# Kernel tuning notes

Measured on AMD Instinct MI355X. Metric: run time of the kernel, lower is better.

## Reference

```python
import jax, jax.numpy as jnp
import numpy as np

K = 20          # knn neighbors (args.k)
BN_EPS = 1e-5   # torch BatchNorm default
LN_EPS = 1e-6


def _bn(x, g, b, axes):
    # training-mode batchnorm over `axes`, channel dim = 1
    m = x.mean(axes, keepdims=True)
    v = x.var(axes, keepdims=True)
    shp = [1] * x.ndim
    shp[1] = x.shape[1]
    return g.reshape(shp) * (x - m) * jax.lax.rsqrt(v + BN_EPS) + b.reshape(shp)


def _lrelu(x):
    return jnp.where(x >= 0, x, 0.2 * x)


def _graph_feature(x, k):
    # x: [B,C,N] -> [B,2C,N,k]  (knn gather + (neighbor-center, center) concat)
    B, C, N = x.shape
    inner = -2.0 * jnp.einsum('bcn,bcm->bnm', x, x)
    xx = jnp.sum(x * x, axis=1)                       # [B,N]
    pd = -xx[:, :, None] - inner - xx[:, None, :]     # negative sq. distance
    idx = jax.lax.top_k(pd, k)[1]                     # [B,N,k]
    xt = jnp.transpose(x, (0, 2, 1))                  # [B,N,C]
    feat = xt[jnp.arange(B)[:, None, None], idx]      # [B,N,k,C] gather
    ctr = xt[:, :, None, :]
    out = jnp.concatenate([feat - ctr, jnp.broadcast_to(ctr, feat.shape)], axis=-1)
    return jnp.transpose(out, (0, 3, 1, 2))


def _conv2d_block(x, w, g, b):
    # 1x1 conv2d (no bias) + BN2d + LeakyReLU(0.2)
    y = jnp.einsum('bcnk,oc->bonk', x, w)
    return _lrelu(_bn(y, g, b, (0, 2, 3)))


def _conv1d_block(x, w, g, b):
    y = jnp.einsum('bcl,oc->bol', x, w)
    return _lrelu(_bn(y, g, b, (0, 2)))


def _squash(t):
    sn = jnp.sum(t * t, axis=-1, keepdims=True)
    return sn * t / ((1.0 + sn) * jnp.sqrt(sn))


def _forward(data, l, dw1, dg1, db1, dw2, dg2, db2, dw3, dg3, db3,
             lin_w, ln_w, ln_b, caps_W,
             cw1, cg1, cb1, cw2, cg2, cb2, cw3, cw4, cg4, cb4, cw5, cg5, cb5):
    B, _, N = data.shape
    # ---- DGCNN encoder ----
    x = _conv2d_block(_graph_feature(data, K), dw1, dg1, db1)
    x1 = x.max(axis=-1)                               # [B,64,N]
    x = _conv2d_block(_graph_feature(x1, K), dw2, dg2, db2)
    x2 = x.max(axis=-1)                               # [B,64,N]
    x = _conv2d_block(_graph_feature(x2, K), dw3, dg3, db3)
    x3 = x.max(axis=-1)                               # [B,128,N]
    feat = jnp.transpose(jnp.concatenate([x1, x2, x3], axis=1), (0, 2, 1))  # [B,N,256]
    h = jnp.einsum('bnc,oc->bno', feat, lin_w)        # [B,N,40]
    mu = h.mean(axis=(1, 2), keepdims=True)
    var = h.var(axis=(1, 2), keepdims=True)
    encoder = jax.nn.relu(ln_w * (h - mu) * jax.lax.rsqrt(var + LN_EPS) + ln_b)  # [B,1024,40]
    # ---- Latent capsule layer (3-iter dynamic routing) ----
    u_hat = jnp.einsum('lpvd,bpd->blpv', caps_W, encoder)  # [B,40,1024,64]
    u_det = jax.lax.stop_gradient(u_hat)
    b_ij = jnp.zeros((B, caps_W.shape[0], caps_W.shape[1]), encoder.dtype)
    v = None
    for it in range(3):
        c = jax.nn.softmax(b_ij, axis=1)
        if it == 2:
            v = _squash(jnp.einsum('blp,blpv->blv', c, u_hat))
        else:
            v = _squash(jnp.einsum('blp,blpv->blv', c, u_det))
            b_ij = b_ij + jnp.einsum('blv,blpv->blp', v, u_det)
    latent = v                                        # [B,40,64]
    # ---- segmentation head ----
    emb = jnp.einsum('bpd,bdv->bpv', encoder, latent) # [B,1024,64]
    emb = emb.max(axis=-1, keepdims=True)             # [B,1024,1]
    lab = _conv1d_block(l.reshape(B, -1, 1), cw1, cg1, cb1)  # [B,64,1]
    emb = jnp.concatenate([emb, lab], axis=1)         # [B,1088,1]
    emb = jnp.tile(emb, (1, 1, N))                    # [B,1088,N]
    emb = jnp.concatenate([emb, jnp.transpose(encoder, (0, 2, 1))], axis=1)  # [B,1128,N]
    r = _conv1d_block(emb, cw2, cg2, cb2)
    r = _conv1d_block(r, cw3, cg2, cb2)               # conv3 shares bn2 params
    r = _conv1d_block(r, cw4, cg4, cb4)
    r = _conv1d_block(r, cw5, cg5, cb5)
    return r                                          # [B,50,N]


def setup_inputs() -> dict:
    key = jax.random.key(0)
    ks = jax.random.split(key, 16)
    B, N = 32, 1024
    f = jnp.float32
    rn = lambda k, s: 0.05 * jax.random.normal(k, s, dtype=f)
    return dict(
        data=jax.random.normal(ks[0], (B, 3, N), dtype=f),
        l=jax.random.uniform(ks[1], (B, 16), dtype=f),
        dw1=rn(ks[2], (64, 6)), dg1=jnp.ones(64, f), db1=jnp.zeros(64, f),
        dw2=rn(ks[3], (64, 128)), dg2=jnp.ones(64, f), db2=jnp.zeros(64, f),
        dw3=rn(ks[4], (128, 128)), dg3=jnp.ones(128, f), db3=jnp.zeros(128, f),
        lin_w=rn(ks[5], (40, 256)),
        ln_w=jnp.ones((N, 40), f), ln_b=jnp.zeros((N, 40), f),
        caps_W=0.01 * jax.random.normal(ks[6], (40, 1024, 64, 40), dtype=f),
        cw1=rn(ks[7], (64, 16)), cg1=jnp.ones(64, f), cb1=jnp.zeros(64, f),
        cw2=rn(ks[8], (256, 1128)), cg2=jnp.ones(256, f), cb2=jnp.zeros(256, f),
        cw3=rn(ks[9], (256, 256)),
        cw4=rn(ks[10], (128, 256)), cg4=jnp.ones(128, f), cb4=jnp.zeros(128, f),
        cw5=rn(ks[11], (50, 128)), cg5=jnp.ones(50, f), cb5=jnp.zeros(50, f),
    )


def reference(data, l, dw1, dg1, db1, dw2, dg2, db2, dw3, dg3, db3,
              lin_w, ln_w, ln_b, caps_W,
              cw1, cg1, cb1, cw2, cg2, cb2, cw3, cw4, cg4, cb4, cw5, cg5, cb5):
    return _forward(data, l, dw1, dg1, db1, dw2, dg2, db2, dw3, dg3, db3,
                    lin_w, ln_w, ln_b, caps_W,
                    cw1, cg1, cb1, cw2, cg2, cb2, cw3, cw4, cg4, cb4, cw5, cg5, cb5)
```

## Files before the change

### kernel.cpp

```cpp
#include <hip/hip_runtime.h>
#include <math.h>

constexpr int NB = 32, NN = 1024, KNN = 20;
constexpr int RTOT = NB * NN;

constexpr size_t SZ_BIG = (size_t)NB * NN * 40 * 64;
constexpr size_t O_BIG  = 0;
constexpr size_t O_XT0  = O_BIG + SZ_BIG;
constexpr size_t O_XT1  = O_XT0 + (size_t)RTOT * 4;
constexpr size_t O_XT2  = O_XT1 + (size_t)RTOT * 64;
constexpr size_t O_XT3  = O_XT2 + (size_t)RTOT * 64;
constexpr size_t O_XX   = O_XT3 + (size_t)RTOT * 128;
constexpr size_t O_IDX  = O_XX + RTOT;
constexpr size_t O_WC1  = O_IDX + (size_t)RTOT * KNN;
constexpr size_t O_WC2  = O_WC1 + 512;
constexpr size_t O_WC3  = O_WC2 + 8192;
constexpr size_t O_LWT  = O_WC3 + 16384;
constexpr size_t O_C2T  = O_LWT + 16384;
constexpr size_t O_C3T  = O_C2T + 10240;
constexpr size_t O_C4T  = O_C3T + 65536;
constexpr size_t O_C5T  = O_C4T + 32768;
constexpr size_t O_H    = O_C5T + 8192;
constexpr size_t O_LNST = O_H + (size_t)RTOT * 64;
constexpr size_t O_BSUM = O_LNST + 64;
constexpr size_t O_BSQ  = O_BSUM + 256;
constexpr size_t O_SCL  = O_BSQ + 256;
constexpr size_t O_SHF  = O_SCL + 256;
constexpr size_t O_SACC = O_SHF + 256;
constexpr size_t O_VB   = O_SACC + 81920;
constexpr size_t O_BIJ  = O_VB + 81920;
constexpr size_t O_EMB  = O_BIJ + (size_t)NB * 40 * NN;
constexpr size_t O_LAB  = O_EMB + RTOT;
constexpr size_t O_BASE = O_LAB + 2048;
constexpr size_t O_PS   = O_BIJ;
constexpr size_t O_PQ   = O_BIJ + 262144;
constexpr size_t O_PB   = O_XT1;
constexpr size_t O_PBU  = O_XT1;

__device__ __forceinline__ float lrelu(float z) { return fmaxf(z, 0.2f * z); }

__device__ __forceinline__ float key2f(unsigned u)
{
    unsigned b = (u & 0x80000000u) ? (u ^ 0x80000000u) : ~u;
    return __uint_as_float(b);
}

__device__ __forceinline__ unsigned bfpack(float a, float b)
{
    unsigned ua = __float_as_uint(a); unsigned ub = __float_as_uint(b);
    ua += 0x7FFFu + ((ua >> 16) & 1u);
    ub += 0x7FFFu + ((ub >> 16) & 1u);
    return (ua >> 16) | (ub & 0xFFFF0000u);
}
__device__ __forceinline__ float bflo(unsigned u) { return __uint_as_float(u << 16); }
__device__ __forceinline__ float bfhi(unsigned u) { return __uint_as_float(u & 0xFFFF0000u); }

__device__ __forceinline__ void wt_do(const float* __restrict__ src, float* __restrict__ dst,
                                      int i, int K, int On, int SS, int coff, int DS, int ooff, int Oreal)
{
    if (i >= K * On) return;
    int c = i / On, o = i - c * On;
    dst[(size_t)c * DS + ooff + o] = (o < Oreal) ? src[(size_t)o * SS + coff + c] : 0.f;
}

__global__ __launch_bounds__(256) void k_wtall(
    const float* __restrict__ dw1, const float* __restrict__ dw2, const float* __restrict__ dw3,
    const float* __restrict__ lw,  const float* __restrict__ cw2, const float* __restrict__ cw3,
    const float* __restrict__ cw4, const float* __restrict__ cw5,
    float* __restrict__ wc1, float* __restrict__ wc2, float* __restrict__ wc3,
    float* __restrict__ lwt, float* __restrict__ c2t, float* __restrict__ c3t,
    float* __restrict__ c4t, float* __restrict__ c5t)
{
    int bid = blockIdx.x, t = threadIdx.x;
    if      (bid < 1)   wt_do(dw1, wc1, (bid - 0) * 256 + t,   3, 64, 6, 0, 128, 0, 64);
    else if (bid < 2)   wt_do(dw1, wc1, (bid - 1) * 256 + t,   3, 64, 6, 3, 128, 64, 64);
    else if (bid < 18)  wt_do(dw2, wc2, (bid - 2) * 256 + t,   64, 64, 128, 0, 128, 0, 64);
    else if (bid < 34)  wt_do(dw2, wc2, (bid - 18) * 256 + t,  64, 64, 128, 64, 128, 64, 64);
    else if (bid < 66)  wt_do(dw3, wc3, (bid - 34) * 256 + t,  64, 128, 128, 0, 256, 0, 128);
    else if (bid < 98)  wt_do(dw3, wc3, (bid - 66) * 256 + t,  64, 128, 128, 64, 256, 128, 128);
    else if (bid < 162) wt_do(lw,  lwt, (bid - 98) * 256 + t,  256, 64, 256, 0, 64, 0, 40);
    else if (bid < 202) wt_do(cw2, c2t, (bid - 162) * 256 + t, 40, 256, 1128, 1088, 256, 0, 256);
    else if (bid < 458) wt_do(cw3, c3t, (bid - 202) * 256 + t, 256, 256, 256, 0, 256, 0, 256);
    else if (bid < 586) wt_do(cw4, c4t, (bid - 458) * 256 + t, 256, 128, 256, 0, 128, 0, 128);
    else                wt_do(cw5, c5t, (bid - 586) * 256 + t, 128, 64, 128, 0, 64, 0, 50);
}

__global__ void k_data_t(const float* __restrict__ d, float* __restrict__ xt,
                         float* __restrict__ xx)
{
    int i = blockIdx.x * 256 + threadIdx.x;
    if (i >= RTOT) return;
    int b = i >> 10, n = i & 1023;
    float s = 0.f;
#pragma unroll
    for (int c = 0; c < 3; ++c) {
        float v = d[((size_t)b * 3 + c) * NN + n];
        xt[(size_t)i * 4 + c] = v;
        s = fmaf(v, v, s);
    }
    xt[(size_t)i * 4 + 3] = 0.f;
    xx[i] = s;
}

template<int CS>
__global__ __launch_bounds__(256) void k_dist(const float* __restrict__ X,
    const float* __restrict__ xx, float* __restrict__ D)
{
    __shared__ float As[16][68];
    __shared__ float Bs[16][68];
    int b = blockIdx.z;
    int r0 = blockIdx.x * 64, m0 = blockIdx.y * 64;
    const float* Xb = X + (size_t)b * NN * CS;
    int t = threadIdx.x;
    int tx = t & 15, ty = t >> 4;
    float acc[4][4] = {};
    for (int k0 = 0; k0 < CS; k0 += 16) {
        __syncthreads();
        {
            int row = t >> 2, kb = (t & 3) * 4;
            float4 a4 = make_float4(0.f, 0.f, 0.f, 0.f);
            float4 b4 = make_float4(0.f, 0.f, 0.f, 0.f);
            if (k0 + kb < CS) {
                a4 = *(const float4*)&Xb[(size_t)(r0 + row) * CS + k0 + kb];
                b4 = *(const float4*)&Xb[(size_t)(m0 + row) * CS + k0 + kb];
            }
            As[kb + 0][row] = a4.x; As[kb + 1][row] = a4.y;
            As[kb + 2][row] = a4.z; As[kb + 3][row] = a4.w;
            Bs[kb + 0][row] = b4.x; Bs[kb + 1][row] = b4.y;
            Bs[kb + 2][row] = b4.z; Bs[kb + 3][row] = b4.w;
        }
        __syncthreads();
#pragma unroll
        for (int k = 0; k < 16; ++k) {
            float4 a = *(const float4*)&As[k][ty * 4];
            float4 bb = *(const float4*)&Bs[k][tx * 4];
            float av[4] = {a.x, a.y, a.z, a.w};
            float bv[4] = {bb.x, bb.y, bb.z, bb.w};
#pragma unroll
            for (int i = 0; i < 4; ++i)
#pragma unroll
                for (int j = 0; j < 4; ++j)
                    acc[i][j] = fmaf(av[i], bv[j], acc[i][j]);
        }
    }
    const float* xxb = xx + b * NN + m0 + tx * 4;
    float x0 = xxb[0], x1 = xxb[1], x2 = xxb[2], x3 = xxb[3];
#pragma unroll
    for (int i = 0; i < 4; ++i) {
        float4 o4 = make_float4(2.f * acc[i][0] - x0, 2.f * acc[i][1] - x1,
                                2.f * acc[i][2] - x2, 2.f * acc[i][3] - x3);
        *(float4*)&D[((size_t)b * NN + r0 + ty * 4 + i) * NN + m0 + tx * 4] = o4;
    }
}

__global__ __launch_bounds__(256) void k_sel(const float* __restrict__ D,
                                             int* __restrict__ idxb)
{
    int gw = blockIdx.x * 4 + (threadIdx.x >> 6);
    int lane = threadIdx.x & 63;
    const float* drow = D + (size_t)gw * NN;
    float vr[16];
#pragma unroll
    for (int j = 0; j < 16; ++j) vr[j] = drow[j * 64 + lane];

    unsigned lo = 0x007FFFFFu;
    unsigned hi = 0xFF800000u;
#pragma unroll 1
    while (hi - lo > 1u) {
        unsigned mid = lo + ((hi - lo) >> 1);
        float tm = key2f(mid);
        int c = 0;
#pragma unroll
        for (int j = 0; j < 16; ++j) c += __popcll(__ballot(vr[j] > tm));
        if (c < KNN) hi = mid; else lo = mid;
    }
    float t = key2f(hi);

    int* outp = idxb + (size_t)gw * KNN;
    unsigned long long mylow = (1ull << lane) - 1ull;
    int base = 0;
#pragma unroll
    for (int j = 0; j < 16; ++j) {
        unsigned long long bmask = __ballot(vr[j] > t);
        if (vr[j] > t) outp[base + __popcll(bmask & mylow)] = j * 64 + lane;
        base += __popcll(bmask);
    }
#pragma unroll 1
    for (int j = 0; j < 16 && base < KNN; ++j) {
        unsigned long long bmask = __ballot(vr[j] == t);
        int pre = __popcll(bmask & mylow);
        if (vr[j] == t && base + pre < KNN) outp[base + pre] = j * 64 + lane;
        base += __popcll(bmask);
    }
}

template<bool ACT, bool BIAS>
__global__ __launch_bounds__(256) void k_gemm(const float* __restrict__ X,
    const float* __restrict__ W, float* __restrict__ Y, int K, int OC, int XS,
    const float* __restrict__ scale, const float* __restrict__ shift,
    const float* __restrict__ bias)
{
    __shared__ float Xs[16][68];
    __shared__ float Ws[16][64];
    int r0 = blockIdx.x * 64, o0 = blockIdx.y * 64;
    int t = threadIdx.x;
    int tx = t & 15, ty = t >> 4;
    float acc[4][4] = {};
    for (int k0 = 0; k0 < K; k0 += 16) {
        __syncthreads();
        {
            int row = t >> 2, kb = (t & 3) * 4;
            float4 xv = make_float4(0.f, 0.f, 0.f, 0.f);
            if (k0 + kb < XS) xv = *(const float4*)&X[(size_t)(r0 + row) * XS + k0 + kb];
            float vv[4] = {xv.x, xv.y, xv.z, xv.w};
#pragma unroll
            for (int u = 0; u < 4; ++u) {
                int k = k0 + kb + u;
                float v = 0.f;
                if (k < K) {
                    v = vv[u];
                    if (ACT) { float z = fmaf(v, scale[k], shift[k]); v = fmaxf(z, 0.2f * z); }
                }
                Xs[kb + u][row] = v;
            }
            int kw = t >> 4, ow = (t & 15) * 4;
            float4 wv = make_float4(0.f, 0.f, 0.f, 0.f);
            if (k0 + kw < K) wv = *(const float4*)&W[(size_t)(k0 + kw) * OC + o0 + ow];
            *(float4*)&Ws[kw][ow] = wv;
        }
        __syncthreads();
#pragma unroll
        for (int k = 0; k < 16; ++k) {
            float4 a = *(const float4*)&Xs[k][ty * 4];
            float4 bb = *(const float4*)&Ws[k][tx * 4];
            float av[4] = {a.x, a.y, a.z, a.w};
            float bvv[4] = {bb.x, bb.y, bb.z, bb.w};
#pragma unroll
            for (int i = 0; i < 4; ++i)
#pragma unroll
                for (int j = 0; j < 4; ++j)
                    acc[i][j] = fmaf(av[i], bvv[j], acc[i][j]);
        }
    }
#pragma unroll
    for (int i = 0; i < 4; ++i) {
        int r = r0 + ty * 4 + i;
        float4 o4;
        float* po = (float*)&o4;
#pragma unroll
        for (int j = 0; j < 4; ++j) {
            float v = acc[i][j];
            if (BIAS) v += bias[(size_t)(r >> 10) * OC + o0 + tx * 4 + j];
            po[j] = v;
        }
        *(float4*)&Y[(size_t)r * OC + o0 + tx * 4] = o4;
    }
}

template<int O>
__global__ __launch_bounds__(256) void k_gather(const float* __restrict__ Z,
    const int* __restrict__ idxb, float* __restrict__ xo,
    float* __restrict__ part_s, float* __restrict__ part_q)
{
    constexpr int OL = O / 64;
    __shared__ float rs[4][O], rq[4][O];
    int b = blockIdx.y, nt = blockIdx.x;
    int t = threadIdx.x, lane = t & 63, w = t >> 6;
    float ps[OL] = {}, pq[OL] = {};
    for (int i = 0; i < 4; ++i) {
        int n = nt * 16 + w * 4 + i;
        size_t r = (size_t)b * NN + n;
        float zd[OL], ym[OL];
#pragma unroll
        for (int j = 0; j < OL; ++j) {
            int o = lane + j * 64;
            zd[j] = Z[r * (2 * O) + O + o] - Z[r * (2 * O) + o];
            ym[j] = -3.4e38f;
        }
        int midx[KNN];
        {
            const int4* ip = (const int4*)&idxb[r * KNN];
#pragma unroll
            for (int q = 0; q < 5; ++q) {
                int4 t4 = ip[q];
                midx[4 * q + 0] = t4.x; midx[4 * q + 1] = t4.y;
                midx[4 * q + 2] = t4.z; midx[4 * q + 3] = t4.w;
            }
        }
#pragma unroll
        for (int k = 0; k < KNN; ++k) {
            size_t rm = (size_t)b * NN + midx[k];
#pragma unroll
            for (int j = 0; j < OL; ++j) {
                float y = Z[rm * (2 * O) + lane + j * 64] + zd[j];
                ym[j] = fmaxf(ym[j], y);
                ps[j] += y; pq[j] = fmaf(y, y, pq[j]);
            }
        }
#pragma unroll
        for (int j = 0; j < OL; ++j) xo[r * O + lane + j * 64] = ym[j];
    }
#pragma unroll
    for (int j = 0; j < OL; ++j) { rs[w][lane + j * 64] = ps[j]; rq[w][lane + j * 64] = pq[j]; }
    __syncthreads();
    if (w == 0) {
        int blk = blockIdx.y * 64 + blockIdx.x;
#pragma unroll
        for (int j = 0; j < OL; ++j) {
            int o = lane + j * 64;
            part_s[(size_t)o * 2048 + blk] = rs[0][o] + rs[1][o] + rs[2][o] + rs[3][o];
            part_q[(size_t)o * 2048 + blk] = rq[0][o] + rq[1][o] + rq[2][o] + rq[3][o];
        }
    }
}

__global__ void k_bnfin2(const float* __restrict__ part_s, const float* __restrict__ part_q,
                         const float* __restrict__ g, const float* __restrict__ bb,
                         float* __restrict__ scale, float* __restrict__ shift,
                         int OC, float invM, float eps)
{
    int o = blockIdx.x * blockDim.x + threadIdx.x;
    if (o >= OC) return;
    const float* ps = part_s + (size_t)o * 2048;
    const float* pq = part_q + (size_t)o * 2048;
    float s0 = 0.f, s1 = 0.f, s2 = 0.f, s3 = 0.f;
    float q0 = 0.f, q1 = 0.f, q2 = 0.f, q3 = 0.f;
    for (int i = 0; i < 2048; i += 4) {
        s0 += ps[i]; s1 += ps[i + 1]; s2 += ps[i + 2]; s3 += ps[i + 3];
        q0 += pq[i]; q1 += pq[i + 1]; q2 += pq[i + 2]; q3 += pq[i + 3];
    }
    float s = (s0 + s1) + (s2 + s3);
    float q = (q0 + q1) + (q2 + q3);
    float mu = s * invM;
    float var = q * invM - mu * mu;
    float sc = g[o] * rsqrtf(var + eps);
    scale[o] = sc; shift[o] = bb[o] - mu * sc;
}

__global__ void k_bnfin3(const float* __restrict__ part_s, const float* __restrict__ part_q,
                         const float* __restrict__ g, const float* __restrict__ bb,
                         float* __restrict__ scale, float* __restrict__ shift,
                         int OC, float invM, float eps)
{
    int o = blockIdx.x * blockDim.x + threadIdx.x;
    if (o >= OC) return;
    const float* ps = part_s + (size_t)o * 128;
    const float* pq = part_q + (size_t)o * 128;
    float s0 = 0.f, s1 = 0.f, s2 = 0.f, s3 = 0.f;
    float q0 = 0.f, q1 = 0.f, q2 = 0.f, q3 = 0.f;
    for (int i = 0; i < 128; i += 4) {
        s0 += ps[i]; s1 += ps[i + 1]; s2 += ps[i + 2]; s3 += ps[i + 3];
        q0 += pq[i]; q1 += pq[i + 1]; q2 += pq[i + 2]; q3 += pq[i + 3];
    }
    float s = (s0 + s1) + (s2 + s3);
    float q = (q0 + q1) + (q2 + q3);
    float mu = s * invM;
    float var = q * invM - mu * mu;
    float sc = g[o] * rsqrtf(var + eps);
    scale[o] = sc; shift[o] = bb[o] - mu * sc;
}

__global__ void k_bnapply(float* __restrict__ x, const float* __restrict__ scale,
                          const float* __restrict__ shift, int total, int O)
{
    int i = blockIdx.x * 256 + threadIdx.x;
    if (i >= total) return;
    int o = i & (O - 1);
    x[i] = lrelu(fmaf(x[i], scale[o], shift[o]));
}

__global__ __launch_bounds__(256) void k_bnapply_rn(float* __restrict__ x,
    const float* __restrict__ scale, const float* __restrict__ shift,
    float* __restrict__ xx)
{
    __shared__ float red[16][17];
    int t = threadIdx.x;
    int i4 = blockIdx.x * 256 + t;
    int q = t & 15, lrow = t >> 4;
    float4 v = ((float4*)x)[i4];
    int o = q * 4;
    v.x = lrelu(fmaf(v.x, scale[o + 0], shift[o + 0]));
    v.y = lrelu(fmaf(v.y, scale[o + 1], shift[o + 1]));
    v.z = lrelu(fmaf(v.z, scale[o + 2], shift[o + 2]));
    v.w = lrelu(fmaf(v.w, scale[o + 3], shift[o + 3]));
    ((float4*)x)[i4] = v;
    float part = fmaf(v.w, v.w, fmaf(v.z, v.z, fmaf(v.y, v.y, v.x * v.x)));
    red[lrow][q] = part;
    __syncthreads();
    if (t < 16) {
        float s = 0.f;
#pragma unroll
        for (int j = 0; j < 16; ++j) s += red[t][j];
        xx[blockIdx.x * 16 + t] = s;
    }
}

__global__ void k_concat(const float* __restrict__ x1, const float* __restrict__ x2,
                         const float* __restrict__ x3, float* __restrict__ f)
{
    int i = blockIdx.x * 256 + threadIdx.x;
    if (i >= RTOT * 256) return;
    int r = i >> 8, c = i & 255;
    float v;
    if (c < 64) v = x1[(size_t)r * 64 + c];
    else if (c < 128) v = x2[(size_t)r * 64 + c - 64];
    else v = x3[(size_t)r * 128 + c - 128];
    f[(size_t)i] = v;
}

__global__ __launch_bounds__(256) void k_lnstats(const float* __restrict__ h, float* __restrict__ st)
{
    __shared__ float rsm[256], rqm[256];
    int b = blockIdx.x, t = threadIdx.x;
    float s = 0.f, q = 0.f;
    for (int i = t; i < 40960; i += 256) {
        int n = i / 40, o = i - n * 40;
        float v = h[((size_t)b * NN + n) * 64 + o];
        s += v; q = fmaf(v, v, q);
    }
    rsm[t] = s; rqm[t] = q; __syncthreads();
    for (int off = 128; off; off >>= 1) {
        if (t < off) { rsm[t] += rsm[t + off]; rqm[t] += rqm[t + off]; }
        __syncthreads();
    }
    if (t == 0) {
        float mu = rsm[0] / 40960.f;
        float var = rqm[0] / 40960.f - mu * mu;
        st[2 * b] = mu; st[2 * b + 1] = rsqrtf(var + 1e-6f);
    }
}

__global__ void k_lnapply(float* __restrict__ h, const float* __restrict__ lnw,
                          const float* __restrict__ lnb, const float* __restrict__ st)
{
    int i = blockIdx.x * 256 + threadIdx.x;
    if (i >= NB * NN * 40) return;
    int b = i / 40960, rem = i - b * 40960, n = rem / 40, o = rem - n * 40;
    float mu = st[2 * b], rstd = st[2 * b + 1];
    size_t a = ((size_t)b * NN + n) * 64 + o;
    float v = fmaf((h[a] - mu) * rstd, lnw[n * 40 + o], lnb[n * 40 + o]);
    h[a] = fmaxf(v, 0.f);
}

__global__ __launch_bounds__(64) void k_uhat(const float* __restrict__ enc,
    const float* __restrict__ caps, unsigned short* __restrict__ U, float* __restrict__ pbu)
{
    __shared__ float clt[40 * 68];
    int pc = blockIdx.x, l = blockIdx.y;
    int lane = threadIdx.x;
    int vg = lane & 7, bg = lane >> 3;
    int v0 = vg * 8, b0 = bg * 4;
    float spart[4][8] = {};
#pragma unroll 1
    for (int pi = 0; pi < 16; ++pi) {
        int p = pc * 16 + pi;
        const float4* cp4 = (const float4*)(caps + ((size_t)l * NN + p) * 2560);
#pragma unroll
        for (int k = 0; k < 10; ++k) {
            int i4 = lane + k * 64;
            float4 cv = cp4[i4];
            int e0 = i4 * 4;
            int v = e0 / 40;
            int d0 = e0 - v * 40;
            clt[(d0 + 0) * 68 + v] = cv.x;
            clt[(d0 + 1) * 68 + v] = cv.y;
            clt[(d0 + 2) * 68 + v] = cv.z;
            clt[(d0 + 3) * 68 + v] = cv.w;
        }
        float acc[4][8] = {};
#pragma unroll
        for (int d4 = 0; d4 < 10; ++d4) {
            float4 e4[4];
#pragma unroll
            for (int i = 0; i < 4; ++i)
                e4[i] = *(const float4*)&enc[((size_t)(b0 + i) * NN + p) * 64 + d4 * 4];
#pragma unroll
            for (int dd = 0; dd < 4; ++dd) {
                int d = d4 * 4 + dd;
                float4 c0 = *(const float4*)&clt[d * 68 + v0];
                float4 c1 = *(const float4*)&clt[d * 68 + v0 + 4];
                float cv[8] = {c0.x, c0.y, c0.z, c0.w, c1.x, c1.y, c1.z, c1.w};
#pragma unroll
                for (int i = 0; i < 4; ++i) {
                    float e = ((const float*)&e4[i])[dd];
#pragma unroll
                    for (int j = 0; j < 8; ++j)
                        acc[i][j] = fmaf(e, cv[j], acc[i][j]);
                }
            }
        }
#pragma unroll
        for (int i = 0; i < 4; ++i) {
            uint4 pk;
            pk.x = bfpack(acc[i][0], acc[i][1]);
            pk.y = bfpack(acc[i][2], acc[i][3]);
            pk.z = bfpack(acc[i][4], acc[i][5]);
            pk.w = bfpack(acc[i][6], acc[i][7]);
            *(uint4*)&U[((size_t)(b0 + i) * NN + p) * 2560 + l * 64 + v0] = pk;
#pragma unroll
            for (int j = 0; j < 8; ++j) spart[i][j] += acc[i][j];
        }
    }
    float* pb = pbu + (size_t)pc * 81920;
#pragma unroll
    for (int i = 0; i < 4; ++i) {
        float4 s0 = make_float4(spart[i][0], spart[i][1], spart[i][2], spart[i][3]);
        float4 s1 = make_float4(spart[i][4], spart[i][5], spart[i][6], spart[i][7]);
        float* dst = &pb[(size_t)(b0 + i) * 2560 + l * 64 + v0];
        *(float4*)dst = s0;
        *(float4*)(dst + 4) = s1;
    }
}

template<int MODE>
__global__ __launch_bounds__(256, 4) void k_route(const unsigned short* __restrict__ U,
    const float* __restrict__ vprev, const float* __restrict__ bin,
    float* __restrict__ bout, float* __restrict__ pbuf)
{
    __shared__ float vl[2560];
    __shared__ float red[4][1280];
    int b = blockIdx.x, pc = blockIdx.y;
    int t = threadIdx.x, lane = t & 63, w = t >> 6;
    for (int i = t; i < 2560; i += 256) vl[i] = vprev[(size_t)b * 2560 + i];
    __syncthreads();
    float4 acc[10];
#pragma unroll
    for (int it = 0; it < 10; ++it) acc[it] = make_float4(0.f, 0.f, 0.f, 0.f);
    int lgrp = lane >> 4;
#pragma unroll 1
    for (int pi = 0; pi < 8; ++pi) {
        int p = pc * 32 + w * 8 + pi;
        const uint2* up2 = (const uint2*)(U + ((size_t)b * NN + p) * 2560);
        uint2 ur[10];
#pragma unroll
        for (int it = 0; it < 10; ++it) ur[it] = up2[it * 64 + lane];
        float pd[10];
#pragma unroll
        for (int it = 0; it < 10; ++it) {
            float4 vv = *(const float4*)&vl[it * 256 + lane * 4];
            float s = bflo(ur[it].x) * vv.x;
            s = fmaf(bfhi(ur[it].x), vv.y, s);
            s = fmaf(bflo(ur[it].y), vv.z, s);
            s = fmaf(bfhi(ur[it].y), vv.w, s);
            s += __shfl_xor(s, 1, 64);
            s += __shfl_xor(s, 2, 64);
            s += __shfl_xor(s, 4, 64);
            s += __shfl_xor(s, 8, 64);
            pd[it] = s;
        }
        if (MODE == 1) {
            if ((lane & 15) == 0) {
#pragma unroll
                for (int it = 0; it < 10; ++it)
                    bout[((size_t)b * 40 + it * 4 + lgrp) * NN + p] = pd[it];
            }
        } else {
#pragma unroll
            for (int it = 0; it < 10; ++it)
                pd[it] += bin[((size_t)b * 40 + it * 4 + lgrp) * NN + p];
        }
        float mx = -3.4e38f;
#pragma unroll
        for (int it = 0; it < 10; ++it) {
            float m = pd[it];
            m = fmaxf(m, __shfl_xor(m, 16, 64));
            m = fmaxf(m, __shfl_xor(m, 32, 64));
            mx = fmaxf(mx, m);
        }
        float eo[10]; float se = 0.f;
#pragma unroll
        for (int it = 0; it < 10; ++it) {
            float e = expf(pd[it] - mx);
            eo[it] = e;
            float sg = e;
            sg += __shfl_xor(sg, 16, 64);
            sg += __shfl_xor(sg, 32, 64);
            se += sg;
        }
        float inv = 1.f / se;
#pragma unroll
        for (int it = 0; it < 10; ++it) {
            float wgt = eo[it] * inv;
            acc[it].x = fmaf(wgt, bflo(ur[it].x), acc[it].x);
            acc[it].y = fmaf(wgt, bfhi(ur[it].x), acc[it].y);
            acc[it].z = fmaf(wgt, bflo(ur[it].y), acc[it].z);
            acc[it].w = fmaf(wgt, bfhi(ur[it].y), acc[it].w);
        }
    }
    float* pb = pbuf + ((size_t)pc * NB + b) * 2560;
#pragma unroll 1
    for (int h = 0; h < 2; ++h) {
        __syncthreads();
#pragma unroll
        for (int it = 0; it < 5; ++it)
            *(float4*)&red[w][it * 256 + lane * 4] = acc[h * 5 + it];
        __syncthreads();
        if (w == 0) {
#pragma unroll
            for (int it = 0; it < 5; ++it) {
                int idx = it * 256 + lane * 4;
                float4 a0 = *(const float4*)&red[0][idx];
                float4 a1 = *(const float4*)&red[1][idx];
                float4 a2 = *(const float4*)&red[2][idx];
                float4 a3 = *(const float4*)&red[3][idx];
                float4 o = make_float4((a0.x + a1.x) + (a2.x + a3.x),
                                       (a0.y + a1.y) + (a2.y + a3.y),
                                       (a0.z + a1.z) + (a2.z + a3.z),
                                       (a0.w + a1.w) + (a2.w + a3.w));
                *(float4*)&pb[h * 1280 + idx] = o;
            }
        }
    }
}

template<int NCH>
__global__ __launch_bounds__(256) void k_sredsq(const float* __restrict__ pbuf,
    float* __restrict__ vout, float premul)
{
    __shared__ float red[16][17];
    __shared__ float fac[16];
    int t = threadIdx.x;
    int i4 = blockIdx.x * 256 + t;
    int q = t & 15, lrow = t >> 4;
    const float4* pb4 = (const float4*)pbuf;
    float4 s = make_float4(0.f, 0.f, 0.f, 0.f);
#pragma unroll 4
    for (int pc = 0; pc < NCH; ++pc) {
        float4 v = pb4[(size_t)pc * (NB * 640) + i4];
        s.x += v.x; s.y += v.y; s.z += v.z; s.w += v.w;
    }
    s.x *= premul; s.y *= premul; s.z *= premul; s.w *= premul;
    float part = fmaf(s.w, s.w, fmaf(s.z, s.z, fmaf(s.y, s.y, s.x * s.x)));
    red[lrow][q] = part;
    __syncthreads();
    if (t < 16) {
        float sn = 0.f;
#pragma unroll
        for (int j = 0; j < 16; ++j) sn += red[t][j];
        fac[t] = sn / ((1.f + sn) * sqrtf(sn));
    }
    __syncthreads();
    float f = fac[lrow];
    ((float4*)vout)[i4] = make_float4(s.x * f, s.y * f, s.z * f, s.w * f);
}

__global__ __launch_bounds__(256) void k_emb(const float* __restrict__ enc,
    const float* __restrict__ lat, float* __restrict__ embm)
{
    __shared__ float latl[2560];
    int b = blockIdx.x, pt = blockIdx.y;
    int t = threadIdx.x, lane = t & 63, w = t >> 6;
    for (int i = t; i < 2560; i += 256) latl[i] = lat[(size_t)b * 2560 + i];
    __syncthreads();
    for (int i = 0; i < 32; ++i) {
        int p = pt * 128 + w * 32 + i;
        const float* ep = enc + ((size_t)b * NN + p) * 64;
        float acc = 0.f;
#pragma unroll
        for (int d = 0; d < 40; ++d) acc = fmaf(ep[d], latl[d * 64 + lane], acc);
        float mx = acc;
#pragma unroll
        for (int s = 32; s; s >>= 1) mx = fmaxf(mx, __shfl_xor(mx, s, 64));
        if (lane == 0) embm[(size_t)b * NN + p] = mx;
    }
}

__global__ __launch_bounds__(256) void k_base2(const float* __restrict__ em,
    const float* __restrict__ lin, const float* __restrict__ cw1,
    const float* __restrict__ cg1, const float* __restrict__ cb1,
    const float* __restrict__ cw2, float* __restrict__ base)
{
    __shared__ float eml[1024];
    __shared__ float lbl[64];
    int b = blockIdx.x, t = threadIdx.x;
    for (int i = t; i < 1024; i += 256) eml[i] = em[(size_t)b * NN + i];
    if (t < 64) {
        int o = t;
        float ys[32]; float s = 0.f, q = 0.f;
#pragma unroll
        for (int bb = 0; bb < 32; ++bb) {
            float y = 0.f;
#pragma unroll
            for (int c = 0; c < 16; ++c) y = fmaf(lin[bb * 16 + c], cw1[o * 16 + c], y);
            ys[bb] = y; s += y; q = fmaf(y, y, q);
        }
        float mu = s / 32.f, var = q / 32.f - mu * mu;
        float sc = cg1[o] * rsqrtf(var + 1e-5f);
        float sh = cb1[o] - mu * sc;
        lbl[o] = lrelu(fmaf(ys[b], sc, sh));
    }
    __syncthreads();
    const float* wr = cw2 + (size_t)t * 1128;
    float acc = 0.f;
    for (int c = 0; c < 1024; ++c) acc = fmaf(wr[c], eml[c], acc);
#pragma unroll
    for (int c = 0; c < 64; ++c) acc = fmaf(wr[1024 + c], lbl[c], acc);
    base[b * 256 + t] = acc;
}

__global__ __launch_bounds__(256) void k_colstats2(const float* __restrict__ Y,
    float* __restrict__ part_s, float* __restrict__ part_q, int OC)
{
    __shared__ float rs[4][64], rq[4][64];
    int chunk = blockIdx.x, o0 = blockIdx.y * 64;
    int t = threadIdx.x, lane = t & 63, w = t >> 6;
    int o = o0 + lane;
    float s = 0.f, q = 0.f;
    for (int j = 0; j < 64; ++j) {
        int r = chunk * 256 + w * 64 + j;
        float v = Y[(size_t)r * OC + o];
        s += v; q = fmaf(v, v, q);
    }
    rs[w][lane] = s; rq[w][lane] = q;
    __syncthreads();
    if (w == 0) {
        part_s[(size_t)o * 128 + chunk] = rs[0][lane] + rs[1][lane] + rs[2][lane] + rs[3][lane];
        part_q[(size_t)o * 128 + chunk] = rq[0][lane] + rq[1][lane] + rq[2][lane] + rq[3][lane];
    }
}

__global__ void k_out(const float* __restrict__ Y, const float* __restrict__ scale,
                      const float* __restrict__ shift, float* __restrict__ out)
{
    int i = blockIdx.x * 256 + threadIdx.x;
    if (i >= NB * 50 * NN) return;
    int n = i & 1023, rest = i >> 10;
    int o = rest % 50, b = rest / 50;
    float y = Y[((size_t)b * NN + n) * 64 + o];
    out[i] = lrelu(fmaf(y, scale[o], shift[o]));
}

extern "C" void kernel_launch(void* const* d_in, const int* in_sizes, int n_in,
                              void* d_out, int out_size, void* d_ws, size_t ws_size,
                              hipStream_t stream)
{
    const float* data = (const float*)d_in[0];
    const float* lin  = (const float*)d_in[1];
    const float* dw1  = (const float*)d_in[2];
    const float* dg1  = (const float*)d_in[3];
    const float* db1  = (const float*)d_in[4];
    const float* dw2  = (const float*)d_in[5];
    const float* dg2  = (const float*)d_in[6];
    const float* db2  = (const float*)d_in[7];
    const float* dw3  = (const float*)d_in[8];
    const float* dg3  = (const float*)d_in[9];
    const float* db3  = (const float*)d_in[10];
    const float* lw   = (const float*)d_in[11];
    const float* lnw  = (const float*)d_in[12];
    const float* lnb  = (const float*)d_in[13];
    const float* caps = (const float*)d_in[14];
    const float* cw1  = (const float*)d_in[15];
    const float* cg1  = (const float*)d_in[16];
    const float* cb1  = (const float*)d_in[17];
    const float* cw2  = (const float*)d_in[18];
    const float* cg2  = (const float*)d_in[19];
    const float* cb2  = (const float*)d_in[20];
    const float* cw3  = (const float*)d_in[21];
    const float* cw4  = (const float*)d_in[22];
    const float* cg4  = (const float*)d_in[23];
    const float* cb4  = (const float*)d_in[24];
    const float* cw5  = (const float*)d_in[25];
    const float* cg5  = (const float*)d_in[26];
    const float* cb5  = (const float*)d_in[27];
    float* out = (float*)d_out;
    float* ws = (float*)d_ws;

    float* big  = ws + O_BIG;
    float* xt0  = ws + O_XT0;
    float* xt1  = ws + O_XT1;
    float* xt2  = ws + O_XT2;
    float* xt3  = ws + O_XT3;
    float* xxp  = ws + O_XX;
    int*   idxb = (int*)(ws + O_IDX);
    float* wc1  = ws + O_WC1;
    float* wc2  = ws + O_WC2;
    float* wc3  = ws + O_WC3;
    float* lwt  = ws + O_LWT;
    float* c2t  = ws + O_C2T;
    float* c3t  = ws + O_C3T;
    float* c4t  = ws + O_C4T;
    float* c5t  = ws + O_C5T;
    float* hbuf = ws + O_H;
    float* lnst = ws + O_LNST;
    float* scl  = ws + O_SCL;
    float* shf  = ws + O_SHF;
    float* vb   = ws + O_VB;
    float* bij  = ws + O_BIJ;
    float* embm = ws + O_EMB;
    float* basep= ws + O_BASE;
    float* psP  = ws + O_PS;
    float* pqP  = ws + O_PQ;
    float* pbuf = ws + O_PB;
    float* pbu  = ws + O_PBU;
    float* Dbuf = big;
    float* Z    = big;
    unsigned short* U = (unsigned short*)big;
    float* yb1  = big;
    float* yb2  = big + 8388608;

    k_wtall<<<618, 256, 0, stream>>>(dw1, dw2, dw3, lw, cw2, cw3, cw4, cw5,
                                     wc1, wc2, wc3, lwt, c2t, c3t, c4t, c5t);
    k_data_t<<<128, 256, 0, stream>>>(data, xt0, xxp);

    k_dist<4><<<dim3(16, 16, 32), 256, 0, stream>>>(xt0, xxp, Dbuf);
    k_sel<<<8192, 256, 0, stream>>>(Dbuf, idxb);
    k_gemm<false, false><<<dim3(512, 2), 256, 0, stream>>>(xt0, wc1, Z, 3, 128, 4, nullptr, nullptr, nullptr);
    k_gather<64><<<dim3(64, 32), 256, 0, stream>>>(Z, idxb, xt1, psP, pqP);
    k_bnfin2<<<1, 64, 0, stream>>>(psP, pqP, dg1, db1, scl, shf, 64, 1.f / 655360.f, 1e-5f);
    k_bnapply_rn<<<2048, 256, 0, stream>>>(xt1, scl, shf, xxp);

    k_dist<64><<<dim3(16, 16, 32), 256, 0, stream>>>(xt1, xxp, Dbuf);
    k_sel<<<8192, 256, 0, stream>>>(Dbuf, idxb);
    k_gemm<false, false><<<dim3(512, 2), 256, 0, stream>>>(xt1, wc2, Z, 64, 128, 64, nullptr, nullptr, nullptr);
    k_gather<64><<<dim3(64, 32), 256, 0, stream>>>(Z, idxb, xt2, psP, pqP);
    k_bnfin2<<<1, 64, 0, stream>>>(psP, pqP, dg2, db2, scl, shf, 64, 1.f / 655360.f, 1e-5f);
    k_bnapply_rn<<<2048, 256, 0, stream>>>(xt2, scl, shf, xxp);

    k_dist<64><<<dim3(16, 16, 32), 256, 0, stream>>>(xt2, xxp, Dbuf);
    k_sel<<<8192, 256, 0, stream>>>(Dbuf, idxb);
    k_gemm<false, false><<<dim3(512, 4), 256, 0, stream>>>(xt2, wc3, Z, 64, 256, 64, nullptr, nullptr, nullptr);
    k_gather<128><<<dim3(64, 32), 256, 0, stream>>>(Z, idxb, xt3, psP, pqP);
    k_bnfin2<<<1, 128, 0, stream>>>(psP, pqP, dg3, db3, scl, shf, 128, 1.f / 655360.f, 1e-5f);
    k_bnapply<<<16384, 256, 0, stream>>>(xt3, scl, shf, RTOT * 128, 128);

    k_concat<<<32768, 256, 0, stream>>>(xt1, xt2, xt3, big);
    k_gemm<false, false><<<dim3(512, 1), 256, 0, stream>>>(big, lwt, hbuf, 256, 64, 256, nullptr, nullptr, nullptr);
    k_lnstats<<<32, 256, 0, stream>>>(hbuf, lnst);
    k_lnapply<<<5120, 256, 0, stream>>>(hbuf, lnw, lnb, lnst);

    k_uhat<<<dim3(64, 40), 64, 0, stream>>>(hbuf, caps, U, pbu);
    k_sredsq<64><<<80, 256, 0, stream>>>(pbu, vb, 1.f / 40.f);
    k_route<1><<<dim3(32, 32), 256, 0, stream>>>(U, vb, nullptr, bij, pbuf);
    k_sredsq<32><<<80, 256, 0, stream>>>(pbuf, vb, 1.f);
    k_route<2><<<dim3(32, 32), 256, 0, stream>>>(U, vb, bij, nullptr, pbuf);
    k_sredsq<32><<<80, 256, 0, stream>>>(pbuf, vb, 1.f);

    k_emb<<<dim3(32, 8), 256, 0, stream>>>(hbuf, vb, embm);
    k_base2<<<32, 256, 0, stream>>>(embm, lin, cw1, cg1, cb1, cw2, basep);

    k_gemm<false, true><<<dim3(512, 4), 256, 0, stream>>>(hbuf, c2t, yb1, 40, 256, 64, nullptr, nullptr, basep);
    k_colstats2<<<dim3(128, 4), 256, 0, stream>>>(yb1, psP, pqP, 256);
    k_bnfin3<<<1, 256, 0, stream>>>(psP, pqP, cg2, cb2, scl, shf, 256, 1.f / 32768.f, 1e-5f);

    k_gemm<true, false><<<dim3(512, 4), 256, 0, stream>>>(yb1, c3t, yb2, 256, 256, 256, scl, shf, nullptr);
    k_colstats2<<<dim3(128, 4), 256, 0, stream>>>(yb2, psP, pqP, 256);
    k_bnfin3<<<1, 256, 0, stream>>>(psP, pqP, cg2, cb2, scl, shf, 256, 1.f / 32768.f, 1e-5f);

    k_gemm<true, false><<<dim3(512, 2), 256, 0, stream>>>(yb2, c4t, yb1, 256, 128, 256, scl, shf, nullptr);
    k_colstats2<<<dim3(128, 2), 256, 0, stream>>>(yb1, psP, pqP, 128);
    k_bnfin3<<<1, 256, 0, stream>>>(psP, pqP, cg4, cb4, scl, shf, 128, 1.f / 32768.f, 1e-5f);

    k_gemm<true, false><<<dim3(512, 1), 256, 0, stream>>>(yb1, c5t, yb2, 128, 64, 128, scl, shf, nullptr);
    k_colstats2<<<dim3(128, 1), 256, 0, stream>>>(yb2, psP, pqP, 64);
    k_bnfin3<<<1, 256, 0, stream>>>(psP, pqP, cg5, cb5, scl, shf, 50, 1.f / 32768.f, 1e-5f);

    k_out<<<6400, 256, 0, stream>>>(yb2, scl, shf, out);
}
```

Measured before the change: 1.528 ms.

## Fuse kNN distance computation with top-k selection in shared memory

```diff
diff --git a/kernel.cpp b/kernel.cpp
--- a/kernel.cpp
+++ b/kernel.cpp
@@ -103,94 +103,77 @@
 }
 
 template<int CS>
-__global__ __launch_bounds__(256) void k_dist(const float* __restrict__ X,
-    const float* __restrict__ xx, float* __restrict__ D)
-{
-    __shared__ float As[16][68];
-    __shared__ float Bs[16][68];
-    int b = blockIdx.z;
-    int r0 = blockIdx.x * 64, m0 = blockIdx.y * 64;
+__global__ __launch_bounds__(256) void k_dsel2(const float* __restrict__ X,
+    const float* __restrict__ xx, int* __restrict__ idxb)
+{
+    __shared__ float dist[8][1024];
+    __shared__ float xmt[64][CS + 1];
+    __shared__ float rows8[8][CS + 1];
+    int b = blockIdx.y, n0 = blockIdx.x * 8;
+    int t = threadIdx.x, lane = t & 63, w = t >> 6;
     const float* Xb = X + (size_t)b * NN * CS;
-    int t = threadIdx.x;
-    int tx = t & 15, ty = t >> 4;
-    float acc[4][4] = {};
-    for (int k0 = 0; k0 < CS; k0 += 16) {
+    for (int i = t; i < 8 * CS; i += 256)
+        rows8[i / CS][i % CS] = Xb[(size_t)(n0 + i / CS) * CS + (i % CS)];
+    const float* xxb = xx + b * NN;
+#pragma unroll 1
+    for (int mt = 0; mt < 16; ++mt) {
         __syncthreads();
-        {
-            int row = t >> 2, kb = (t & 3) * 4;
-            float4 a4 = make_float4(0.f, 0.f, 0.f, 0.f);
-            float4 b4 = make_float4(0.f, 0.f, 0.f, 0.f);
-            if (k0 + kb < CS) {
-                a4 = *(const float4*)&Xb[(size_t)(r0 + row) * CS + k0 + kb];
-                b4 = *(const float4*)&Xb[(size_t)(m0 + row) * CS + k0 + kb];
-            }
-            As[kb + 0][row] = a4.x; As[kb + 1][row] = a4.y;
-            As[kb + 2][row] = a4.z; As[kb + 3][row] = a4.w;
-            Bs[kb + 0][row] = b4.x; Bs[kb + 1][row] = b4.y;
-            Bs[kb + 2][row] = b4.z; Bs[kb + 3][row] = b4.w;
+        for (int i4 = t; i4 < 64 * CS / 4; i4 += 256) {
+            int e0 = i4 * 4;
+            int m = e0 / CS, c = e0 % CS;
+            float4 v = *(const float4*)&Xb[(size_t)(mt * 64 + m) * CS + c];
+            xmt[m][c + 0] = v.x; xmt[m][c + 1] = v.y;
+            xmt[m][c + 2] = v.z; xmt[m][c + 3] = v.w;
         }
         __syncthreads();
-#pragma unroll
-        for (int k = 0; k < 16; ++k) {
-            float4 a = *(const float4*)&As[k][ty * 4];
-            float4 bb = *(const float4*)&Bs[k][tx * 4];
-            float av[4] = {a.x, a.y, a.z, a.w};
-            float bv[4] = {bb.x, bb.y, bb.z, bb.w};
-#pragma unroll
-            for (int i = 0; i < 4; ++i)
-#pragma unroll
-                for (int j = 0; j < 4; ++j)
-                    acc[i][j] = fmaf(av[i], bv[j], acc[i][j]);
-        }
-    }
-    const float* xxb = xx + b * NN + m0 + tx * 4;
-    float x0 = xxb[0], x1 = xxb[1], x2 = xxb[2], x3 = xxb[3];
-#pragma unroll
-    for (int i = 0; i < 4; ++i) {
-        float4 o4 = make_float4(2.f * acc[i][0] - x0, 2.f * acc[i][1] - x1,
-                                2.f * acc[i][2] - x2, 2.f * acc[i][3] - x3);
-        *(float4*)&D[((size_t)b * NN + r0 + ty * 4 + i) * NN + m0 + tx * 4] = o4;
-    }
-}
-
-__global__ __launch_bounds__(256) void k_sel(const float* __restrict__ D,
-                                             int* __restrict__ idxb)
-{
-    int gw = blockIdx.x * 4 + (threadIdx.x >> 6);
-    int lane = threadIdx.x & 63;
-    const float* drow = D + (size_t)gw * NN;
-    float vr[16];
-#pragma unroll
-    for (int j = 0; j < 16; ++j) vr[j] = drow[j * 64 + lane];
-
-    unsigned lo = 0x007FFFFFu;
-    unsigned hi = 0xFF800000u;
+        int m = mt * 64 + lane;
+        float acc0 = 0.f, acc1 = 0.f;
+#pragma unroll
+        for (int c = 0; c < CS; ++c) {
+            float xv = xmt[lane][c];
+            acc0 = fmaf(rows8[2 * w][c], xv, acc0);
+            acc1 = fmaf(rows8[2 * w + 1][c], xv, acc1);
+        }
+        float xxm = xxb[m];
+        dist[2 * w][m] = 2.f * acc0 - xxm;
+        dist[2 * w + 1][m] = 2.f * acc1 - xxm;
+    }
 #pragma unroll 1
-    while (hi - lo > 1u) {
-        unsigned mid = lo + ((hi - lo) >> 1);
-        float tm = key2f(mid);
-        int c = 0;
-#pragma unroll
-        for (int j = 0; j < 16; ++j) c += __popcll(__ballot(vr[j] > tm));
-        if (c < KNN) hi = mid; else lo = mid;
-    }
-    float t = key2f(hi);
-
-    int* outp = idxb + (size_t)gw * KNN;
-    unsigned long long mylow = (1ull << lane) - 1ull;
-    int base = 0;
-#pragma unroll
-    for (int j = 0; j < 16; ++j) {
-        unsigned long long bmask = __ballot(vr[j] > t);
-        if (vr[j] > t) outp[base + __popcll(bmask & mylow)] = j * 64 + lane;
-        base += __popcll(bmask);
-    }
+    for (int rr = 0; rr < 2; ++rr) {
+        int row = 2 * w + rr;
+        float vr[16];
+#pragma unroll
+        for (int j = 0; j < 16; ++j) vr[j] = dist[row][j * 64 + lane];
+
+        unsigned lo = 0x007FFFFFu;
+        unsigned hi = 0xFF800000u;
 #pragma unroll 1
-    for (int j = 0; j < 16 && base < KNN; ++j) {
-        unsigned long long bmask = __ballot(vr[j] == t);
-        int pre = __popcll(bmask & mylow);
-        if (vr[j] == t && base + pre < KNN) outp[base + pre] = j * 64 + lane;
-        base += __popcll(bmask);
+        while (hi - lo > 1u) {
+            unsigned mid = lo + ((hi - lo) >> 1);
+            float tm = key2f(mid);
+            int c = 0;
+#pragma unroll
+            for (int j = 0; j < 16; ++j) c += __popcll(__ballot(vr[j] > tm));
+            if (c < KNN) hi = mid; else lo = mid;
+        }
+        float tv = key2f(hi);
+
+        int* outp = idxb + ((size_t)b * NN + n0 + row) * KNN;
+        unsigned long long mylow = (1ull << lane) - 1ull;
+        int base = 0;
+#pragma unroll
+        for (int j = 0; j < 16; ++j) {
+            unsigned long long bmask = __ballot(vr[j] > tv);
+            if (vr[j] > tv) outp[base + __popcll(bmask & mylow)] = j * 64 + lane;
+            base += __popcll(bmask);
+        }
+#pragma unroll 1
+        for (int j = 0; j < 16 && base < KNN; ++j) {
+            unsigned long long bmask = __ballot(vr[j] == tv);
+            int pre = __popcll(bmask & mylow);
+            if (vr[j] == tv && base + pre < KNN) outp[base + pre] = j * 64 + lane;
+            base += __popcll(bmask);
+        }
     }
 }
 
@@ -792,7 +775,6 @@
     float* pqP  = ws + O_PQ;
     float* pbuf = ws + O_PB;
     float* pbu  = ws + O_PBU;
-    float* Dbuf = big;
     float* Z    = big;
     unsigned short* U = (unsigned short*)big;
     float* yb1  = big;
@@ -802,22 +784,19 @@
                                      wc1, wc2, wc3, lwt, c2t, c3t, c4t, c5t);
     k_data_t<<<128, 256, 0, stream>>>(data, xt0, xxp);
 
-    k_dist<4><<<dim3(16, 16, 32), 256, 0, stream>>>(xt0, xxp, Dbuf);
-    k_sel<<<8192, 256, 0, stream>>>(Dbuf, idxb);
+    k_dsel2<4><<<dim3(128, 32), 256, 0, stream>>>(xt0, xxp, idxb);
     k_gemm<false, false><<<dim3(512, 2), 256, 0, stream>>>(xt0, wc1, Z, 3, 128, 4, nullptr, nullptr, nullptr);
     k_gather<64><<<dim3(64, 32), 256, 0, stream>>>(Z, idxb, xt1, psP, pqP);
     k_bnfin2<<<1, 64, 0, stream>>>(psP, pqP, dg1, db1, scl, shf, 64, 1.f / 655360.f, 1e-5f);
     k_bnapply_rn<<<2048, 256, 0, stream>>>(xt1, scl, shf, xxp);
 
-    k_dist<64><<<dim3(16, 16, 32), 256, 0, stream>>>(xt1, xxp, Dbuf);
-    k_sel<<<8192, 256, 0, stream>>>(Dbuf, idxb);
+    k_dsel2<64><<<dim3(128, 32), 256, 0, stream>>>(xt1, xxp, idxb);
     k_gemm<false, false><<<dim3(512, 2), 256, 0, stream>>>(xt1, wc2, Z, 64, 128, 64, nullptr, nullptr, nullptr);
     k_gather<64><<<dim3(64, 32), 256, 0, stream>>>(Z, idxb, xt2, psP, pqP);
     k_bnfin2<<<1, 64, 0, stream>>>(psP, pqP, dg2, db2, scl, shf, 64, 1.f / 655360.f, 1e-5f);
     k_bnapply_rn<<<2048, 256, 0, stream>>>(xt2, scl, shf, xxp);
 
-    k_dist<64><<<dim3(16, 16, 32), 256, 0, stream>>>(xt2, xxp, Dbuf);
-    k_sel<<<8192, 256, 0, stream>>>(Dbuf, idxb);
+    k_dsel2<64><<<dim3(128, 32), 256, 0, stream>>>(xt2, xxp, idxb);
     k_gemm<false, false><<<dim3(512, 4), 256, 0, stream>>>(xt2, wc3, Z, 64, 256, 64, nullptr, nullptr, nullptr);
     k_gather<128><<<dim3(64, 32), 256, 0, stream>>>(Z, idxb, xt3, psP, pqP);
     k_bnfin2<<<1, 128, 0, stream>>>(psP, pqP, dg3, db3, scl, shf, 128, 1.f / 655360.f, 1e-5f);
```

Measured after the change: 1.843 ms. 1.21x slower.
